# Kernel tuning notes

Hardware: AMD Instinct MI355X
Metric: run time of the kernel (lower is better)

## Reference

```python
import jax, jax.numpy as jnp
import numpy as np

R = 1          # radius
EPS = 0.01
K = 2 * R + 1  # box kernel size


def boxfilter(x):
    """Replication-pad by R, then depthwise KxK mean filter (groups=C)."""
    xp = jnp.pad(x, ((0, 0), (0, 0), (R, R), (R, R)), mode='edge')
    c = x.shape[1]
    k = jnp.full((c, 1, K, K), 1.0 / (K * K), dtype=x.dtype)
    return jax.lax.conv_general_dilated(
        xp, k, window_strides=(1, 1), padding='VALID',
        feature_group_count=c,
        dimension_numbers=('NCHW', 'OIHW', 'NCHW'))


def _interp_axis(arr, n_in, n_out, axis):
    # bilinear with align_corners=True along one axis
    pos = jnp.linspace(0.0, n_in - 1.0, n_out)
    i0 = jnp.floor(pos).astype(jnp.int32)
    i1 = jnp.minimum(i0 + 1, n_in - 1)
    t = (pos - i0).astype(arr.dtype)
    a0 = jnp.take(arr, i0, axis=axis)
    a1 = jnp.take(arr, i1, axis=axis)
    shp = [1] * arr.ndim
    shp[axis] = n_out
    t = t.reshape(shp)
    return a0 * (1 - t) + a1 * t


def upsample_bilinear(x, H, W):
    _, _, h, w = x.shape
    x = _interp_axis(x, h, H, 2)
    x = _interp_axis(x, w, W, 3)
    return x


def setup_inputs() -> dict:
    key = jax.random.key(0)
    k1, k2, k3 = jax.random.split(key, 3)
    x_lr = jax.random.uniform(k1, (4, 3, 512, 512), dtype=jnp.float32)
    y_lr = jax.random.uniform(k2, (4, 3, 512, 512), dtype=jnp.float32)
    x_hr = jax.random.uniform(k3, (4, 3, 2048, 2048), dtype=jnp.float32)
    return {'x_lr': x_lr, 'y_lr': y_lr, 'x_hr': x_hr}


def reference(x_lr, y_lr, x_hr):
    H, W = x_hr.shape[2], x_hr.shape[3]
    mean_x = boxfilter(x_lr)
    mean_y = boxfilter(y_lr)
    cov_xy = boxfilter(x_lr * y_lr) - mean_x * mean_y
    var_x = boxfilter(x_lr * x_lr) - mean_x * mean_x
    A = cov_xy / (var_x + EPS)
    b = mean_y - A * mean_x
    mean_A = upsample_bilinear(boxfilter(A), H, W)
    mean_b = upsample_bilinear(boxfilter(b), H, W)
    res = jnp.clip(mean_A * x_hr + mean_b, 0.0, 255.0)
    return res.astype(jnp.float32)
```

## Files before the change

kernel.cpp:

```cpp
#include <hip/hip_runtime.h>

#define RAD   1
#define EPS_F 0.01f
#define LR_H  512
#define LR_W  512
#define HR_H  2048
#define HR_W  2048
#define NC    12

#define LR_PLANE (LR_H * LR_W)
#define HR_PLANE (HR_H * HR_W)
#define LR_TOTAL (NC * LR_PLANE)
#define HR_TOTAL (NC * HR_PLANE)

__global__ void __launch_bounds__(256) k_compute_Ab(
    const float* __restrict__ x, const float* __restrict__ y,
    float* __restrict__ A, float* __restrict__ b) {
    int idx = blockIdx.x * blockDim.x + threadIdx.x;
    if (idx >= LR_TOTAL) return;
    int w = idx & (LR_W - 1);
    int h = (idx >> 9) & (LR_H - 1);
    int plane = idx >> 18;
    const float* xp = x + (size_t)plane * LR_PLANE;
    const float* yp = y + (size_t)plane * LR_PLANE;

    float sx = 0.f, sy = 0.f, sxy = 0.f, sxx = 0.f;
#pragma unroll
    for (int di = -1; di <= 1; ++di) {
        int hh = min(max(h + di, 0), LR_H - 1);
        int rowoff = hh * LR_W;
#pragma unroll
        for (int dj = -1; dj <= 1; ++dj) {
            int ww = min(max(w + dj, 0), LR_W - 1);
            float xv = xp[rowoff + ww];
            float yv = yp[rowoff + ww];
            sx  += xv;
            sy  += yv;
            sxy += xv * yv;
            sxx += xv * xv;
        }
    }
    const float inv9 = 1.0f / 9.0f;
    float mx  = sx  * inv9;
    float my  = sy  * inv9;
    float cov = sxy * inv9 - mx * my;
    float var = sxx * inv9 - mx * mx;
    float Av  = cov / (var + EPS_F);
    float bv  = my - Av * mx;
    A[idx] = Av;
    b[idx] = bv;
}

__global__ void __launch_bounds__(256) k_box_Ab(
    const float* __restrict__ A, const float* __restrict__ b,
    float* __restrict__ mA, float* __restrict__ mb) {
    int idx = blockIdx.x * blockDim.x + threadIdx.x;
    if (idx >= LR_TOTAL) return;
    int w = idx & (LR_W - 1);
    int h = (idx >> 9) & (LR_H - 1);
    int plane = idx >> 18;
    const float* Ap = A + (size_t)plane * LR_PLANE;
    const float* bp = b + (size_t)plane * LR_PLANE;

    float sA = 0.f, sB = 0.f;
#pragma unroll
    for (int di = -1; di <= 1; ++di) {
        int hh = min(max(h + di, 0), LR_H - 1);
        int rowoff = hh * LR_W;
#pragma unroll
        for (int dj = -1; dj <= 1; ++dj) {
            int ww = min(max(w + dj, 0), LR_W - 1);
            sA += Ap[rowoff + ww];
            sB += bp[rowoff + ww];
        }
    }
    const float inv9 = 1.0f / 9.0f;
    mA[idx] = sA * inv9;
    mb[idx] = sB * inv9;
}

__global__ void __launch_bounds__(256) k_upsample_fuse(
    const float* __restrict__ mA, const float* __restrict__ mb,
    const float* __restrict__ xhr, float* __restrict__ out) {
    int vid = blockIdx.x * blockDim.x + threadIdx.x;
    if (vid >= HR_TOTAL / 4) return;
    int idx = vid * 4;
    int j0base = idx & (HR_W - 1);
    int i      = (idx >> 11) & (HR_H - 1);
    int plane  = idx >> 22;

    const float scale_h = (float)(LR_H - 1) / (float)(HR_H - 1);
    const float scale_w = (float)(LR_W - 1) / (float)(HR_W - 1);

    float ph = i * scale_h;
    int   i0 = (int)floorf(ph);
    int   i1 = min(i0 + 1, LR_H - 1);
    float th = ph - (float)i0;

    const float* Ap = mA + (size_t)plane * LR_PLANE;
    const float* bp = mb + (size_t)plane * LR_PLANE;
    const float4 xv = *(const float4*)(xhr + idx);
    float4 r;

    float res[4];
    float xin[4] = {xv.x, xv.y, xv.z, xv.w};
#pragma unroll
    for (int k = 0; k < 4; ++k) {
        int jj = j0base + k;
        float pw = jj * scale_w;
        int   j0 = (int)floorf(pw);
        int   j1 = min(j0 + 1, LR_W - 1);
        float tw = pw - (float)j0;

        float a_l = Ap[i0 * LR_W + j0] * (1.f - th) + Ap[i1 * LR_W + j0] * th;
        float a_r = Ap[i0 * LR_W + j1] * (1.f - th) + Ap[i1 * LR_W + j1] * th;
        float a_v = a_l * (1.f - tw) + a_r * tw;

        float b_l = bp[i0 * LR_W + j0] * (1.f - th) + bp[i1 * LR_W + j0] * th;
        float b_r = bp[i0 * LR_W + j1] * (1.f - th) + bp[i1 * LR_W + j1] * th;
        float b_v = b_l * (1.f - tw) + b_r * tw;

        float v = a_v * xin[k] + b_v;
        res[k] = fminf(fmaxf(v, 0.0f), 255.0f);
    }
    r.x = res[0]; r.y = res[1]; r.z = res[2]; r.w = res[3];
    *(float4*)(out + idx) = r;
}

extern "C" void kernel_launch(void* const* d_in, const int* in_sizes, int n_in,
                              void* d_out, int out_size, void* d_ws, size_t ws_size,
                              hipStream_t stream) {
    const float* x_lr = (const float*)d_in[0];
    const float* y_lr = (const float*)d_in[1];
    const float* x_hr = (const float*)d_in[2];
    float* out = (float*)d_out;

    float* A  = (float*)d_ws;
    float* b  = A  + LR_TOTAL;
    float* mA = b  + LR_TOTAL;
    float* mb = mA + LR_TOTAL;

    {
        int threads = 256;
        int blocks = (LR_TOTAL + threads - 1) / threads;
        k_compute_Ab<<<blocks, threads, 0, stream>>>(x_lr, y_lr, A, b);
        k_box_Ab<<<blocks, threads, 0, stream>>>(A, b, mA, mb);
    }
    {
        int threads = 256;
        int blocks = (HR_TOTAL / 4 + threads - 1) / threads;
        k_upsample_fuse<<<blocks, threads, 0, stream>>>(mA, mb, x_hr, out);
    }
}
```

Before: 378.5 us.

## Stage vertically interpolated low-res row in shared memory per output row

Each block now handles one high-res output row. It first interpolates the two needed low-res rows of mean_A and mean_b vertically into shared memory, padded by one entry to handle the right edge. Threads then do only the horizontal lerp from LDS while streaming x_hr and out as float4. This removes the eight redundant global gathers per output pixel and the per-pixel vertical blend, at the cost of a __syncthreads and a fixed row-per-block mapping.

Measured after the change: 372.2 us. About the same (-1.7%).

```diff
diff --git a/kernel.cpp b/kernel.cpp
--- a/kernel.cpp
+++ b/kernel.cpp
@@ -82,49 +82,60 @@
 __global__ void __launch_bounds__(256) k_upsample_fuse(
     const float* __restrict__ mA, const float* __restrict__ mb,
     const float* __restrict__ xhr, float* __restrict__ out) {
-    int vid = blockIdx.x * blockDim.x + threadIdx.x;
-    if (vid >= HR_TOTAL / 4) return;
-    int idx = vid * 4;
-    int j0base = idx & (HR_W - 1);
-    int i      = (idx >> 11) & (HR_H - 1);
-    int plane  = idx >> 22;
+    __shared__ float hA[513];
+    __shared__ float hb[513];
 
-    const float scale_h = (float)(LR_H - 1) / (float)(HR_H - 1);
-    const float scale_w = (float)(LR_W - 1) / (float)(HR_W - 1);
+    int bid = blockIdx.x;
+    int i     = bid & (HR_H - 1);
+    int plane = bid >> 11;
 
-    float ph = i * scale_h;
-    int   i0 = (int)floorf(ph);
+    const float scale = (float)(LR_H - 1) / (float)(HR_H - 1);
+
+    float ph = i * scale;
+    int   i0 = (int)ph;
     int   i1 = min(i0 + 1, LR_H - 1);
     float th = ph - (float)i0;
+    float omh = 1.0f - th;
 
     const float* Ap = mA + (size_t)plane * LR_PLANE;
     const float* bp = mb + (size_t)plane * LR_PLANE;
-    const float4 xv = *(const float4*)(xhr + idx);
-    float4 r;
+    int tid = threadIdx.x;
 
-    float res[4];
-    float xin[4] = {xv.x, xv.y, xv.z, xv.w};
+    for (int c = tid; c < 513; c += 256) {
+        int col = min(c, LR_W - 1);
+        float a0 = Ap[i0 * LR_W + col];
+        float a1 = Ap[i1 * LR_W + col];
+        float b0 = bp[i0 * LR_W + col];
+        float b1 = bp[i1 * LR_W + col];
+        hA[c] = a0 * omh + a1 * th;
+        hb[c] = b0 * omh + b1 * th;
+    }
+    __syncthreads();
+
+    const float* xrow = xhr + (size_t)plane * HR_PLANE + (size_t)i * HR_W;
+    float*       orow = out + (size_t)plane * HR_PLANE + (size_t)i * HR_W;
+
 #pragma unroll
-    for (int k = 0; k < 4; ++k) {
-        int jj = j0base + k;
-        float pw = jj * scale_w;
-        int   j0 = (int)floorf(pw);
-        int   j1 = min(j0 + 1, LR_W - 1);
-        float tw = pw - (float)j0;
-
-        float a_l = Ap[i0 * LR_W + j0] * (1.f - th) + Ap[i1 * LR_W + j0] * th;
-        float a_r = Ap[i0 * LR_W + j1] * (1.f - th) + Ap[i1 * LR_W + j1] * th;
-        float a_v = a_l * (1.f - tw) + a_r * tw;
-
-        float b_l = bp[i0 * LR_W + j0] * (1.f - th) + bp[i1 * LR_W + j0] * th;
-        float b_r = bp[i0 * LR_W + j1] * (1.f - th) + bp[i1 * LR_W + j1] * th;
-        float b_v = b_l * (1.f - tw) + b_r * tw;
-
-        float v = a_v * xin[k] + b_v;
-        res[k] = fminf(fmaxf(v, 0.0f), 255.0f);
+    for (int g = 0; g < 2; ++g) {
+        int j = (tid + g * 256) * 4;
+        const float4 xv = *(const float4*)(xrow + j);
+        float xin[4] = {xv.x, xv.y, xv.z, xv.w};
+        float r[4];
+#pragma unroll
+        for (int k = 0; k < 4; ++k) {
+            float pw = (float)(j + k) * scale;
+            int   j0 = (int)pw;
+            float tw = pw - (float)j0;
+            float omw = 1.0f - tw;
+            float a  = hA[j0] * omw + hA[j0 + 1] * tw;
+            float bb = hb[j0] * omw + hb[j0 + 1] * tw;
+            float v  = a * xin[k] + bb;
+            r[k] = fminf(fmaxf(v, 0.0f), 255.0f);
+        }
+        float4 o;
+        o.x = r[0]; o.y = r[1]; o.z = r[2]; o.w = r[3];
+        *(float4*)(orow + j) = o;
     }
-    r.x = res[0]; r.y = res[1]; r.z = res[2]; r.w = res[3];
-    *(float4*)(out + idx) = r;
 }
 
 extern "C" void kernel_launch(void* const* d_in, const int* in_sizes, int n_in,
@@ -148,7 +159,7 @@
     }
     {
         int threads = 256;
-        int blocks = (HR_TOTAL / 4 + threads - 1) / threads;
+        int blocks = NC * HR_H;
         k_upsample_fuse<<<blocks, threads, 0, stream>>>(mA, mb, x_hr, out);
     }
 }
```
